# Kernel tuning notes

Measured on AMD Instinct MI355X. Metric: run time of the kernel, lower is better.

The kernel has to match this reference:

```python
import jax, jax.numpy as jnp
import numpy as np
from jax.ops import segment_sum, segment_max

N, E, IN_DIM, HID, HEADS, B, ACTIONS = 16384, 262144, 512, 256, 4, 64, 32
NEG_SLOPE = 0.2  # PyG GATConv default leaky-relu slope


def setup_inputs() -> dict:
    key = jax.random.key(0)
    ks = jax.random.split(key, 12)
    x = jax.random.normal(ks[0], (N, IN_DIM), dtype=jnp.float32)
    edge_index = jax.random.randint(ks[1], (2, E), 0, N, dtype=jnp.int64)
    batch = jnp.sort(jax.random.randint(ks[2], (N,), 0, B, dtype=jnp.int64))
    s = 0.05
    return {
        "x": x,
        "edge_index": edge_index,
        "batch": batch,
        # SAGEConv: lin_l (neighbors, with bias) + lin_r (root, no bias)
        "sage_w_l": jax.random.normal(ks[3], (IN_DIM, HID), dtype=jnp.float32) * s,
        "sage_b_l": jnp.zeros((HID,), dtype=jnp.float32),
        "sage_w_r": jax.random.normal(ks[4], (IN_DIM, HID), dtype=jnp.float32) * s,
        # GATConv: shared lin, per-head attention vectors, output bias (concat=False)
        "gat_w": jax.random.normal(ks[5], (HID, HEADS * HID), dtype=jnp.float32) * s,
        "gat_att_src": jax.random.normal(ks[6], (HEADS, HID), dtype=jnp.float32) * s,
        "gat_att_dst": jax.random.normal(ks[7], (HEADS, HID), dtype=jnp.float32) * s,
        "gat_b": jnp.zeros((HID,), dtype=jnp.float32),
        # action head
        "head_w": jax.random.normal(ks[8], (HID, ACTIONS), dtype=jnp.float32) * s,
        "head_b": jnp.zeros((ACTIONS,), dtype=jnp.float32),
    }


def reference(x, edge_index, batch, sage_w_l, sage_b_l, sage_w_r,
              gat_w, gat_att_src, gat_att_dst, gat_b, head_w, head_b):
    src, dst = edge_index[0], edge_index[1]

    # ---- SAGEConv (mean aggregation): lin_l(mean_j x_j) + lin_r(x_i) ----
    agg = segment_sum(x[src], dst, num_segments=N)                 # [N, IN_DIM]
    deg = segment_sum(jnp.ones((E,), x.dtype), dst, num_segments=N)
    mean_nbr = agg / jnp.maximum(deg, 1.0)[:, None]
    h = mean_nbr @ sage_w_l + sage_b_l + x @ sage_w_r              # [N, HID]
    h = jax.nn.relu(h)
    # dropout is identity at inference (training=False)

    # ---- GATConv (adds self-loops, concat=False -> head average) ----
    loop = jnp.arange(N, dtype=src.dtype)
    si = jnp.concatenate([src, loop])                              # [E2]
    di = jnp.concatenate([dst, loop])
    g = (h @ gat_w).reshape(N, HEADS, HID)                         # [N, H, C]
    a_src = jnp.einsum('nhc,hc->nh', g, gat_att_src)               # [N, H]
    a_dst = jnp.einsum('nhc,hc->nh', g, gat_att_dst)
    logits = jax.nn.leaky_relu(a_src[si] + a_dst[di], NEG_SLOPE)   # [E2, H]
    m = segment_max(logits, di, num_segments=N)                    # per-target max
    ex = jnp.exp(logits - m[di])
    denom = segment_sum(ex, di, num_segments=N)
    alpha = ex / denom[di]                                         # [E2, H]
    out = segment_sum(g[si] * alpha[:, :, None], di, num_segments=N)  # [N, H, C]
    out = jax.nn.relu(out.mean(axis=1) + gat_b)                    # [N, HID]

    # ---- global mean pool + action head ----
    pooled = segment_sum(out, batch, num_segments=B)
    cnt = segment_sum(jnp.ones((N,), out.dtype), batch, num_segments=B)
    pooled = pooled / jnp.maximum(cnt, 1.0)[:, None]               # [B, HID]
    return pooled @ head_w + head_b                                # [B, ACTIONS]
```

## Files before the change

kernel.cpp:

```cpp
#include <hip/hip_runtime.h>
#include <math.h>

#define N_NODES 16384
#define N_EDGES 262144
#define IN_DIM  512
#define HID     256
#define HEADS   4
#define NBATCH  64
#define ACTIONS 32
#define NEG_SLOPE 0.2f

typedef __attribute__((ext_vector_type(8))) short short8;
typedef __attribute__((ext_vector_type(4))) float f32x4;

__device__ __forceinline__ float lrelu(float v) { return v > 0.f ? v : NEG_SLOPE * v; }

__device__ __forceinline__ unsigned short bf16_rne(float f) {
    union { float f; unsigned int u; } x; x.f = f;
    unsigned int u = x.u;
    unsigned int r = (u + 0x7FFFu + ((u >> 16) & 1u)) >> 16;
    return (unsigned short)r;
}

__device__ __forceinline__ float bf16_to_f32(unsigned short s) {
    union { unsigned int u; float f; } x; x.u = (unsigned int)s << 16;
    return x.f;
}

__device__ __forceinline__ float4 bf4_to_f4(ushort4 u) {
    return make_float4(bf16_to_f32(u.x), bf16_to_f32(u.y), bf16_to_f32(u.z), bf16_to_f32(u.w));
}

__device__ __forceinline__ void async_copy16(const unsigned short* g, unsigned short* l) {
    __builtin_amdgcn_global_load_lds(
        (const __attribute__((address_space(1))) unsigned int*)g,
        (__attribute__((address_space(3))) unsigned int*)l, 16, 0, 0);
}

#define NB_WLR  1024
#define NB_WSTK 1024
#define NB_WATT 8
#define NB_DEG  1024
#define NB_SETUP (NB_WLR + NB_WSTK + NB_WATT + NB_DEG)

__global__ __launch_bounds__(256) void setup_kernel(
        const float* __restrict__ wl, const float* __restrict__ wr, unsigned short* __restrict__ bt1,
        const float* __restrict__ gat_w, unsigned short* __restrict__ bt2,
        const float* __restrict__ att_src, const float* __restrict__ att_dst, float* __restrict__ watt,
        const int* __restrict__ ei, int* __restrict__ deg) {
    int bid = blockIdx.x, tid = threadIdx.x;
    if (bid < NB_WLR) {
        int idx = bid * 256 + tid;
        int j = idx >> 9;
        int k = idx & 511;
        float v = (j < HID) ? wl[k * HID + j] : wr[k * HID + (j - HID)];
        bt1[idx] = bf16_rne(v);
    } else if (bid < NB_WLR + NB_WSTK) {
        int idx = (bid - NB_WLR) * 256 + tid;
        int c = idx >> 10;
        int r = idx & 1023;
        int h = r >> 8;
        int k = r & 255;
        bt2[idx] = bf16_rne(gat_w[(size_t)k * (HEADS * HID) + h * HID + c]);
    } else if (bid < NB_WLR + NB_WSTK + NB_WATT) {
        int j = bid - NB_WLR - NB_WSTK;
        int c = tid;
        int hh = j & 3;
        const float* att = (j < 4) ? (att_src + hh * HID) : (att_dst + hh * HID);
        float s = 0.f;
        for (int cc = 0; cc < HID; cc++)
            s += gat_w[(size_t)c * (HEADS * HID) + hh * HID + cc] * att[cc];
        watt[j * HID + c] = s;
    } else {
        int e = (bid - NB_WLR - NB_WSTK - NB_WATT) * 256 + tid;
        if (e < N_EDGES) atomicAdd(&deg[ei[N_EDGES + e]], 1);
    }
}

__global__ __launch_bounds__(256) void scan_kernel(const int* __restrict__ deg,
                                                   int* __restrict__ row_start,
                                                   int* __restrict__ pos) {
    int t = threadIdx.x;
    int lane = t & 63, wv = t >> 6;
    int base = t * 64;
    int4 buf[16];
    int sum = 0;
#pragma unroll
    for (int i = 0; i < 16; i++) {
        buf[i] = ((const int4*)(deg + base))[i];
        sum += buf[i].x + buf[i].y + buf[i].z + buf[i].w;
    }
    int v = sum;
#pragma unroll
    for (int off = 1; off < 64; off <<= 1) {
        int u = __shfl_up(v, off);
        if (lane >= off) v += u;
    }
    __shared__ int wsum[4];
    if (lane == 63) wsum[wv] = v;
    __syncthreads();
    int wbase = 0;
    for (int w0 = 0; w0 < wv; w0++) wbase += wsum[w0];
    int run = wbase + v - sum;
#pragma unroll
    for (int i = 0; i < 16; i++) {
        int4 b = buf[i];
        int4 o;
        o.x = run; run += b.x;
        o.y = run; run += b.y;
        o.z = run; run += b.z;
        o.w = run; run += b.w;
        ((int4*)(row_start + base))[i] = o;
        ((int4*)(pos + base))[i] = o;
    }
    if (t == 255) row_start[N_NODES] = run;
}

__global__ void fill_kernel(const int* __restrict__ ei, int* __restrict__ pos,
                            int* __restrict__ col) {
    int e = blockIdx.x * 256 + threadIdx.x;
    if (e < N_EDGES) {
        int s = ei[e];
        int d = ei[N_EDGES + e];
        int p = atomicAdd(&pos[d], 1);
        col[p] = s;
    }
}

#define BK 32

__global__ __launch_bounds__(256) void gemm1_kernel(const float* __restrict__ X,
                                                    const unsigned short* __restrict__ Bt,
                                                    unsigned short* __restrict__ Cb,
                                                    int Nn, int K) {
    __shared__ __align__(16) unsigned short As[2][2][64 * BK];
    __shared__ __align__(16) unsigned short Bs[2][2][128 * BK];

    int tid  = threadIdx.x;
    int wv   = tid >> 6;
    int lane = tid & 63;
    int m0 = blockIdx.y * 64;
    int n0 = blockIdx.x * 128;
    int wm = (wv & 1) * 32;
    int wn = (wv >> 1) * 64;

    int srow = tid >> 2;
    int scol = (tid & 3) * 8;
    const float*          Xg  = X  + (size_t)(m0 + srow) * K + scol;
    const unsigned short* Bg0 = Bt + (size_t)(n0 + srow) * K + scol;
    const unsigned short* Bg1 = Bt + (size_t)(n0 + 64 + srow) * K + scol;

    int fr = lane & 15;
    int fk = (lane >> 4) * 8;
    f32x4 acc[2][4] = {};
    float4 pa0[2], pa1[2];

#pragma unroll
    for (int s = 0; s < 2; s++) {
        int ko = s * BK;
        async_copy16(Bg0 + ko, &Bs[0][s][wv * 512]);
        async_copy16(Bg1 + ko, &Bs[0][s][2048 + wv * 512]);
        pa0[s] = *(const float4*)(Xg + ko);
        pa1[s] = *(const float4*)(Xg + ko + 4);
    }
#pragma unroll
    for (int s = 0; s < 2; s++) {
        short8 p;
        p[0] = (short)bf16_rne(pa0[s].x); p[1] = (short)bf16_rne(pa0[s].y);
        p[2] = (short)bf16_rne(pa0[s].z); p[3] = (short)bf16_rne(pa0[s].w);
        p[4] = (short)bf16_rne(pa1[s].x); p[5] = (short)bf16_rne(pa1[s].y);
        p[6] = (short)bf16_rne(pa1[s].z); p[7] = (short)bf16_rne(pa1[s].w);
        *(short8*)&As[0][s][srow * BK + scol] = p;
    }
    __syncthreads();

    int cur = 0;
    for (int kt = 0; kt < K; kt += 2 * BK) {
        int nxt = kt + 2 * BK;
        bool pf = nxt < K;
        if (pf) {
#pragma unroll
            for (int s = 0; s < 2; s++) {
                int ko = nxt + s * BK;
                async_copy16(Bg0 + ko, &Bs[cur ^ 1][s][wv * 512]);
                async_copy16(Bg1 + ko, &Bs[cur ^ 1][s][2048 + wv * 512]);
                pa0[s] = *(const float4*)(Xg + ko);
                pa1[s] = *(const float4*)(Xg + ko + 4);
            }
        }

#pragma unroll
        for (int s = 0; s < 2; s++) {
            short8 af[2], bf[4];
#pragma unroll
            for (int mi = 0; mi < 2; mi++)
                af[mi] = *(const short8*)&As[cur][s][(wm + mi * 16 + fr) * BK + fk];
#pragma unroll
            for (int ni = 0; ni < 4; ni++)
                bf[ni] = *(const short8*)&Bs[cur][s][(wn + ni * 16 + fr) * BK + fk];
#pragma unroll
            for (int mi = 0; mi < 2; mi++)
#pragma unroll
                for (int ni = 0; ni < 4; ni++)
                    acc[mi][ni] = __builtin_amdgcn_mfma_f32_16x16x32_bf16(af[mi], bf[ni], acc[mi][ni], 0, 0, 0);
        }

        if (pf) {
#pragma unroll
            for (int s = 0; s < 2; s++) {
                short8 p;
                p[0] = (short)bf16_rne(pa0[s].x); p[1] = (short)bf16_rne(pa0[s].y);
                p[2] = (short)bf16_rne(pa0[s].z); p[3] = (short)bf16_rne(pa0[s].w);
                p[4] = (short)bf16_rne(pa1[s].x); p[5] = (short)bf16_rne(pa1[s].y);
                p[6] = (short)bf16_rne(pa1[s].z); p[7] = (short)bf16_rne(pa1[s].w);
                *(short8*)&As[cur ^ 1][s][srow * BK + scol] = p;
            }
        }
        __syncthreads();
        cur ^= 1;
    }

    int cr = (lane >> 4) * 4;
    int cc = lane & 15;
#pragma unroll
    for (int mi = 0; mi < 2; mi++) {
#pragma unroll
        for (int ni = 0; ni < 4; ni++) {
            int gc = n0 + wn + ni * 16 + cc;
#pragma unroll
            for (int r = 0; r < 4; r++) {
                int gr = m0 + wm + mi * 16 + cr + r;
                Cb[(size_t)gr * Nn + gc] = bf16_rne(acc[mi][ni][r]);
            }
        }
    }
}

__global__ __launch_bounds__(256) void gemm2_pool_kernel(const unsigned short* __restrict__ A,
                                                         const unsigned short* __restrict__ Bt,
                                                         const int* __restrict__ batch,
                                                         const float* __restrict__ bias,
                                                         float scale,
                                                         float* __restrict__ pooled,
                                                         int Nn, int K) {
    __shared__ __align__(16) unsigned short As[2][2][64 * BK];
    __shared__ __align__(16) unsigned short Bs[2][2][64 * BK];
    __shared__ int bsh[64];

    int tid  = threadIdx.x;
    int wv   = tid >> 6;
    int lane = tid & 63;
    int m0 = blockIdx.y * 64;
    int n0 = blockIdx.x * 64;
    int wm = (wv & 1) * 32;
    int wn = (wv >> 1) * 32;

    if (tid < 64) bsh[tid] = batch[m0 + tid];

    int srow = tid >> 2;
    int scol = (tid & 3) * 8;
    const unsigned short* Ag = A  + (size_t)(m0 + srow) * K + scol;
    const unsigned short* Bg = Bt + (size_t)(n0 + srow) * K + scol;

    int fr = lane & 15;
    int fk = (lane >> 4) * 8;
    f32x4 acc[2][2] = {};

#pragma unroll
    for (int s = 0; s < 2; s++) {
        int ko = s * BK;
        async_copy16(Ag + ko, &As[0][s][wv * 512]);
        async_copy16(Bg + ko, &Bs[0][s][wv * 512]);
    }
    __syncthreads();

    int cur = 0;
    for (int kt = 0; kt < K; kt += 2 * BK) {
        int nxt = kt + 2 * BK;
        bool pf = nxt < K;
        if (pf) {
#pragma unroll
            for (int s = 0; s < 2; s++) {
                int ko = nxt + s * BK;
                async_copy16(Ag + ko, &As[cur ^ 1][s][wv * 512]);
                async_copy16(Bg + ko, &Bs[cur ^ 1][s][wv * 512]);
            }
        }

#pragma unroll
        for (int s = 0; s < 2; s++) {
            short8 af[2], bf[2];
#pragma unroll
            for (int mi = 0; mi < 2; mi++)
                af[mi] = *(const short8*)&As[cur][s][(wm + mi * 16 + fr) * BK + fk];
#pragma unroll
            for (int ni = 0; ni < 2; ni++)
                bf[ni] = *(const short8*)&Bs[cur][s][(wn + ni * 16 + fr) * BK + fk];
#pragma unroll
            for (int mi = 0; mi < 2; mi++)
#pragma unroll
                for (int ni = 0; ni < 2; ni++)
                    acc[mi][ni] = __builtin_amdgcn_mfma_f32_16x16x32_bf16(af[mi], bf[ni], acc[mi][ni], 0, 0, 0);
        }
        __syncthreads();
        cur ^= 1;
    }

    int cr = (lane >> 4) * 4;
    int cc = lane & 15;
#pragma unroll
    for (int mi = 0; mi < 2; mi++) {
        int rowb = wm + mi * 16 + cr;
        int b0 = bsh[rowb], b3 = bsh[rowb + 3];
#pragma unroll
        for (int ni = 0; ni < 2; ni++) {
            int gc = n0 + wn + ni * 16 + cc;
            float b = bias[gc];
            float v0 = fmaxf(fmaf(acc[mi][ni][0], scale, b), 0.f);
            float v1 = fmaxf(fmaf(acc[mi][ni][1], scale, b), 0.f);
            float v2 = fmaxf(fmaf(acc[mi][ni][2], scale, b), 0.f);
            float v3 = fmaxf(fmaf(acc[mi][ni][3], scale, b), 0.f);
            if (b0 == b3) {
                atomicAdd(&pooled[b0 * HID + gc], (v0 + v1) + (v2 + v3));
            } else {
                atomicAdd(&pooled[bsh[rowb + 0] * HID + gc], v0);
                atomicAdd(&pooled[bsh[rowb + 1] * HID + gc], v1);
                atomicAdd(&pooled[bsh[rowb + 2] * HID + gc], v2);
                atomicAdd(&pooled[bsh[rowb + 3] * HID + gc], v3);
            }
        }
    }
}

__global__ __launch_bounds__(256) void sage_agg_kernel(const unsigned short* __restrict__ xlr,
                                                       const int* __restrict__ row_start,
                                                       const int* __restrict__ col,
                                                       const float* __restrict__ b_l,
                                                       const float* __restrict__ watt,
                                                       unsigned short* __restrict__ hb,
                                                       float* __restrict__ a_att) {
    __shared__ float watt_s[8 * HID];
    for (int i = threadIdx.x; i < 8 * HID; i += 256) watt_s[i] = watt[i];
    __syncthreads();

    int wave = threadIdx.x >> 6;
    int lane = threadIdx.x & 63;
    int n = blockIdx.x * 4 + wave;
    int start = row_start[n], end = row_start[n + 1];
    int c0 = lane * 4;

    float4 acc = make_float4(0.f, 0.f, 0.f, 0.f);
    int e = start;
    for (; e + 4 <= end; e += 4) {
        int s0 = col[e], s1 = col[e + 1], s2 = col[e + 2], s3 = col[e + 3];
        ushort4 u0 = *(const ushort4*)(xlr + (size_t)s0 * IN_DIM + c0);
        ushort4 u1 = *(const ushort4*)(xlr + (size_t)s1 * IN_DIM + c0);
        ushort4 u2 = *(const ushort4*)(xlr + (size_t)s2 * IN_DIM + c0);
        ushort4 u3 = *(const ushort4*)(xlr + (size_t)s3 * IN_DIM + c0);
        float4 v0 = bf4_to_f4(u0), v1 = bf4_to_f4(u1), v2 = bf4_to_f4(u2), v3 = bf4_to_f4(u3);
        acc.x += (v0.x + v1.x) + (v2.x + v3.x);
        acc.y += (v0.y + v1.y) + (v2.y + v3.y);
        acc.z += (v0.z + v1.z) + (v2.z + v3.z);
        acc.w += (v0.w + v1.w) + (v2.w + v3.w);
    }
    for (; e < end; e++) {
        int s = col[e];
        float4 v = bf4_to_f4(*(const ushort4*)(xlr + (size_t)s * IN_DIM + c0));
        acc.x += v.x; acc.y += v.y; acc.z += v.z; acc.w += v.w;
    }
    float inv = 1.f / (float)max(end - start, 1);
    float4 xr = bf4_to_f4(*(const ushort4*)(xlr + (size_t)n * IN_DIM + HID + c0));
    float4 bl = *(const float4*)(b_l + c0);
    float4 hv;
    hv.x = fmaxf(fmaf(acc.x, inv, bl.x + xr.x), 0.f);
    hv.y = fmaxf(fmaf(acc.y, inv, bl.y + xr.y), 0.f);
    hv.z = fmaxf(fmaf(acc.z, inv, bl.z + xr.z), 0.f);
    hv.w = fmaxf(fmaf(acc.w, inv, bl.w + xr.w), 0.f);
    ushort4 ho;
    ho.x = bf16_rne(hv.x); ho.y = bf16_rne(hv.y); ho.z = bf16_rne(hv.z); ho.w = bf16_rne(hv.w);
    *(ushort4*)(hb + (size_t)n * HID + c0) = ho;

    float p[8];
#pragma unroll
    for (int j = 0; j < 8; j++) {
        float4 wt = *(const float4*)&watt_s[j * HID + c0];
        p[j] = hv.x * wt.x + hv.y * wt.y + hv.z * wt.z + hv.w * wt.w;
    }
#pragma unroll
    for (int off = 32; off; off >>= 1)
#pragma unroll
        for (int j = 0; j < 8; j++) p[j] += __shfl_down(p[j], off);
    if (lane == 0) {
#pragma unroll
        for (int j = 0; j < 8; j++) a_att[n * 8 + j] = p[j];
    }
}

__global__ __launch_bounds__(256) void gat_agg_kernel(const unsigned short* __restrict__ hb,
                                                      const float* __restrict__ a_att,
                                                      const int* __restrict__ row_start,
                                                      const int* __restrict__ col,
                                                      unsigned short* __restrict__ T) {
    __shared__ __align__(16) float w_s[4][64 * 4];
    int wave = threadIdx.x >> 6;
    int lane = threadIdx.x & 63;
    int n = blockIdx.x * 4 + wave;
    int start = row_start[n], end = row_start[n + 1];

    float4 an = *(const float4*)(a_att + n * 8);
    float4 ad = *(const float4*)(a_att + n * 8 + 4);
    float adst[4] = {ad.x, ad.y, ad.z, ad.w};
    float selfl[4] = {lrelu(an.x + ad.x), lrelu(an.y + ad.y), lrelu(an.z + ad.z), lrelu(an.w + ad.w)};
    float m[4], wself[4];
#pragma unroll
    for (int hh = 0; hh < 4; hh++) {
        m[hh] = fmaxf(selfl[hh], 0.f);
        wself[hh] = __expf(selfl[hh] - m[hh]);
    }

    int c0 = lane * 4;
    float4 hn = bf4_to_f4(*(const ushort4*)(hb + (size_t)n * HID + c0));
    float4 acc[4];
#pragma unroll
    for (int hh = 0; hh < 4; hh++)
        acc[hh] = make_float4(wself[hh] * hn.x, wself[hh] * hn.y, wself[hh] * hn.z, wself[hh] * hn.w);

    float dpart[4] = {0.f, 0.f, 0.f, 0.f};

    for (int base = start; base < end; base += 64) {
        int cnt = min(64, end - base);
        if (lane < cnt) {
            int s = col[base + lane];
            float4 as = *(const float4*)(a_att + s * 8);
            float4 wv;
            wv.x = __expf(lrelu(as.x + adst[0]) - m[0]);
            wv.y = __expf(lrelu(as.y + adst[1]) - m[1]);
            wv.z = __expf(lrelu(as.z + adst[2]) - m[2]);
            wv.w = __expf(lrelu(as.w + adst[3]) - m[3]);
            *(float4*)&w_s[wave][lane * 4] = wv;
            dpart[0] += wv.x; dpart[1] += wv.y; dpart[2] += wv.z; dpart[3] += wv.w;
        }
        __builtin_amdgcn_wave_barrier();

        int i = 0;
        for (; i + 2 <= cnt; i += 2) {
            int s0 = col[base + i], s1 = col[base + i + 1];
            float4 w0 = *(const float4*)&w_s[wave][i * 4];
            float4 w1 = *(const float4*)&w_s[wave][(i + 1) * 4];
            ushort4 u0 = *(const ushort4*)(hb + (size_t)s0 * HID + c0);
            ushort4 u1 = *(const ushort4*)(hb + (size_t)s1 * HID + c0);
            float4 h0 = bf4_to_f4(u0), h1 = bf4_to_f4(u1);
            float wr0[4] = {w0.x, w0.y, w0.z, w0.w};
            float wr1[4] = {w1.x, w1.y, w1.z, w1.w};
#pragma unroll
            for (int hh = 0; hh < 4; hh++) {
                acc[hh].x = fmaf(wr0[hh], h0.x, fmaf(wr1[hh], h1.x, acc[hh].x));
                acc[hh].y = fmaf(wr0[hh], h0.y, fmaf(wr1[hh], h1.y, acc[hh].y));
                acc[hh].z = fmaf(wr0[hh], h0.z, fmaf(wr1[hh], h1.z, acc[hh].z));
                acc[hh].w = fmaf(wr0[hh], h0.w, fmaf(wr1[hh], h1.w, acc[hh].w));
            }
        }
        if (i < cnt) {
            int s0 = col[base + i];
            float4 w0 = *(const float4*)&w_s[wave][i * 4];
            float4 h0 = bf4_to_f4(*(const ushort4*)(hb + (size_t)s0 * HID + c0));
            float wr0[4] = {w0.x, w0.y, w0.z, w0.w};
#pragma unroll
            for (int hh = 0; hh < 4; hh++) {
                acc[hh].x = fmaf(wr0[hh], h0.x, acc[hh].x);
                acc[hh].y = fmaf(wr0[hh], h0.y, acc[hh].y);
                acc[hh].z = fmaf(wr0[hh], h0.z, acc[hh].z);
                acc[hh].w = fmaf(wr0[hh], h0.w, acc[hh].w);
            }
        }
        __builtin_amdgcn_wave_barrier();
    }

#pragma unroll
    for (int off = 32; off; off >>= 1)
#pragma unroll
        for (int hh = 0; hh < 4; hh++) dpart[hh] += __shfl_down(dpart[hh], off);
    float invd[4];
#pragma unroll
    for (int hh = 0; hh < 4; hh++)
        invd[hh] = 1.f / (__shfl(dpart[hh], 0) + wself[hh]);

#pragma unroll
    for (int hh = 0; hh < 4; hh++) {
        ushort4 o;
        o.x = bf16_rne(acc[hh].x * invd[hh]); o.y = bf16_rne(acc[hh].y * invd[hh]);
        o.z = bf16_rne(acc[hh].z * invd[hh]); o.w = bf16_rne(acc[hh].w * invd[hh]);
        *(ushort4*)(T + (size_t)n * (HEADS * HID) + hh * HID + c0) = o;
    }
}

__device__ __forceinline__ int lower_bound_i(const int* a, int n, int v) {
    int lo = 0, hi = n;
    while (lo < hi) {
        int mid = (lo + hi) >> 1;
        if (a[mid] < v) lo = mid + 1; else hi = mid;
    }
    return lo;
}

__global__ __launch_bounds__(256) void head_kernel(const float* __restrict__ pooled,
                                                   const int* __restrict__ batch,
                                                   const float* __restrict__ head_w,
                                                   const float* __restrict__ head_b,
                                                   float* __restrict__ out) {
    __shared__ float sm[HID];
    int b = blockIdx.x;
    int c = threadIdx.x;
    int lo = lower_bound_i(batch, N_NODES, b);
    int hi = lower_bound_i(batch, N_NODES, b + 1);
    int cnt = hi - lo;
    sm[c] = pooled[b * HID + c] / (float)max(cnt, 1);
    __syncthreads();
    if (c < ACTIONS) {
        float acc = head_b[c];
        for (int k = 0; k < HID; k++) acc = fmaf(sm[k], head_w[k * ACTIONS + c], acc);
        out[b * ACTIONS + c] = acc;
    }
}

extern "C" void kernel_launch(void* const* d_in, const int* in_sizes, int n_in,
                              void* d_out, int out_size, void* d_ws, size_t ws_size,
                              hipStream_t stream) {
    const float* x        = (const float*)d_in[0];
    const int*   ei       = (const int*)d_in[1];
    const int*   batch    = (const int*)d_in[2];
    const float* sage_w_l = (const float*)d_in[3];
    const float* sage_b_l = (const float*)d_in[4];
    const float* sage_w_r = (const float*)d_in[5];
    const float* gat_w    = (const float*)d_in[6];
    const float* att_src  = (const float*)d_in[7];
    const float* att_dst  = (const float*)d_in[8];
    const float* gat_b    = (const float*)d_in[9];
    const float* head_w   = (const float*)d_in[10];
    const float* head_b   = (const float*)d_in[11];
    float* out = (float*)d_out;

    char* w = (char*)d_ws;
    int*   deg    = (int*)w;   w += (size_t)N_NODES * 4;
    float* pooled = (float*)w; w += (size_t)NBATCH * HID * 4;
    size_t zero_bytes = (size_t)N_NODES * 4 + (size_t)NBATCH * HID * 4;
    float* a_att  = (float*)w; w += (size_t)N_NODES * 8 * 4;
    float* watt   = (float*)w; w += (size_t)8 * HID * 4;
    unsigned short* xlr = (unsigned short*)w; w += (size_t)N_NODES * IN_DIM * 2;
    unsigned short* hb  = (unsigned short*)w; w += (size_t)N_NODES * HID * 2;
    unsigned short* T   = (unsigned short*)w; w += (size_t)N_NODES * HEADS * HID * 2;
    unsigned short* bt1 = (unsigned short*)w; w += (size_t)(2 * HID) * IN_DIM * 2;
    unsigned short* bt2 = (unsigned short*)w; w += (size_t)HID * (HEADS * HID) * 2;
    int* row_start= (int*)w;   w += (size_t)(N_NODES + 64) * 4;
    int* pos      = (int*)w;   w += (size_t)N_NODES * 4;
    int* col      = (int*)w;   w += (size_t)N_EDGES * 4;

    hipMemsetAsync(d_ws, 0, zero_bytes, stream);

    setup_kernel<<<NB_SETUP, 256, 0, stream>>>(sage_w_l, sage_w_r, bt1,
                                               gat_w, bt2, att_src, att_dst, watt,
                                               ei, deg);

    scan_kernel<<<1, 256, 0, stream>>>(deg, row_start, pos);
    fill_kernel<<<N_EDGES / 256, 256, 0, stream>>>(ei, pos, col);

    gemm1_kernel<<<dim3((2 * HID) / 128, N_NODES / 64), 256, 0, stream>>>(
        x, bt1, xlr, 2 * HID, IN_DIM);

    sage_agg_kernel<<<N_NODES / 4, 256, 0, stream>>>(xlr, row_start, col, sage_b_l, watt, hb, a_att);

    gat_agg_kernel<<<N_NODES / 4, 256, 0, stream>>>(hb, a_att, row_start, col, T);

    gemm2_pool_kernel<<<dim3(HID / 64, N_NODES / 64), 256, 0, stream>>>(
        T, bt2, batch, gat_b, 0.25f, pooled, HID, HEADS * HID);

    head_kernel<<<NBATCH, 256, 0, stream>>>(pooled, batch, head_w, head_b, out);
}
```

Baseline: 263.1 us.

## Pre-convert x to bf16 in setup and fuse action head into gemm2 tail

The fp32→bf16 conversion of x moves out of gemm1 and into a dedicated section of the setup kernel, writing into the T buffer before T is needed. This lets gemm1 stream A with async global-to-LDS copies, the same way it already loads B. The separate head kernel is removed. The last gemm2 block, found through an atomic counter, now computes the mean-pool division and the action-head matmul. This saves one launch but adds an extra pass over x and a serial tail done by a single block.

```diff
diff --git a/kernel.cpp b/kernel.cpp
--- a/kernel.cpp
+++ b/kernel.cpp
@@ -37,17 +37,19 @@
         (__attribute__((address_space(3))) unsigned int*)l, 16, 0, 0);
 }
 
-#define NB_WLR  1024
-#define NB_WSTK 1024
-#define NB_WATT 8
-#define NB_DEG  1024
-#define NB_SETUP (NB_WLR + NB_WSTK + NB_WATT + NB_DEG)
+#define NB_WLR   1024
+#define NB_WSTK  1024
+#define NB_WATT  8
+#define NB_DEG   1024
+#define NB_XCONV 4096
+#define NB_SETUP (NB_WLR + NB_WSTK + NB_WATT + NB_DEG + NB_XCONV)
 
 __global__ __launch_bounds__(256) void setup_kernel(
         const float* __restrict__ wl, const float* __restrict__ wr, unsigned short* __restrict__ bt1,
         const float* __restrict__ gat_w, unsigned short* __restrict__ bt2,
         const float* __restrict__ att_src, const float* __restrict__ att_dst, float* __restrict__ watt,
-        const int* __restrict__ ei, int* __restrict__ deg) {
+        const int* __restrict__ ei, int* __restrict__ deg,
+        const float* __restrict__ x, unsigned short* __restrict__ xb) {
     int bid = blockIdx.x, tid = threadIdx.x;
     if (bid < NB_WLR) {
         int idx = bid * 256 + tid;
@@ -71,9 +73,19 @@
         for (int cc = 0; cc < HID; cc++)
             s += gat_w[(size_t)c * (HEADS * HID) + hh * HID + cc] * att[cc];
         watt[j * HID + c] = s;
-    } else {
+    } else if (bid < NB_WLR + NB_WSTK + NB_WATT + NB_DEG) {
         int e = (bid - NB_WLR - NB_WSTK - NB_WATT) * 256 + tid;
         if (e < N_EDGES) atomicAdd(&deg[ei[N_EDGES + e]], 1);
+    } else {
+        size_t idx = (size_t)(bid - NB_WLR - NB_WSTK - NB_WATT - NB_DEG) * 2048 + (size_t)tid * 8;
+        float4 a0 = *(const float4*)(x + idx);
+        float4 a1 = *(const float4*)(x + idx + 4);
+        short8 p;
+        p[0] = (short)bf16_rne(a0.x); p[1] = (short)bf16_rne(a0.y);
+        p[2] = (short)bf16_rne(a0.z); p[3] = (short)bf16_rne(a0.w);
+        p[4] = (short)bf16_rne(a1.x); p[5] = (short)bf16_rne(a1.y);
+        p[6] = (short)bf16_rne(a1.z); p[7] = (short)bf16_rne(a1.w);
+        *(short8*)(xb + idx) = p;
     }
 }
 
@@ -129,7 +141,7 @@
 
 #define BK 32
 
-__global__ __launch_bounds__(256) void gemm1_kernel(const float* __restrict__ X,
+__global__ __launch_bounds__(256) void gemm1_kernel(const unsigned short* __restrict__ Ab,
                                                     const unsigned short* __restrict__ Bt,
                                                     unsigned short* __restrict__ Cb,
                                                     int Nn, int K) {
@@ -146,31 +158,20 @@
 
     int srow = tid >> 2;
     int scol = (tid & 3) * 8;
-    const float*          Xg  = X  + (size_t)(m0 + srow) * K + scol;
+    const unsigned short* Ag  = Ab + (size_t)(m0 + srow) * K + scol;
     const unsigned short* Bg0 = Bt + (size_t)(n0 + srow) * K + scol;
     const unsigned short* Bg1 = Bt + (size_t)(n0 + 64 + srow) * K + scol;
 
     int fr = lane & 15;
     int fk = (lane >> 4) * 8;
     f32x4 acc[2][4] = {};
-    float4 pa0[2], pa1[2];
 
 #pragma unroll
     for (int s = 0; s < 2; s++) {
         int ko = s * BK;
-        async_copy16(Bg0 + ko, &Bs[0][s][wv * 512]);
-        async_copy16(Bg1 + ko, &Bs[0][s][2048 + wv * 512]);
-        pa0[s] = *(const float4*)(Xg + ko);
-        pa1[s] = *(const float4*)(Xg + ko + 4);
-    }
-#pragma unroll
-    for (int s = 0; s < 2; s++) {
-        short8 p;
-        p[0] = (short)bf16_rne(pa0[s].x); p[1] = (short)bf16_rne(pa0[s].y);
-        p[2] = (short)bf16_rne(pa0[s].z); p[3] = (short)bf16_rne(pa0[s].w);
-        p[4] = (short)bf16_rne(pa1[s].x); p[5] = (short)bf16_rne(pa1[s].y);
-        p[6] = (short)bf16_rne(pa1[s].z); p[7] = (short)bf16_rne(pa1[s].w);
-        *(short8*)&As[0][s][srow * BK + scol] = p;
+        async_copy16(Ag + ko,      &As[0][s][wv * 512]);
+        async_copy16(Bg0 + ko,     &Bs[0][s][wv * 512]);
+        async_copy16(Bg1 + ko,     &Bs[0][s][2048 + wv * 512]);
     }
     __syncthreads();
 
@@ -182,10 +183,9 @@
 #pragma unroll
             for (int s = 0; s < 2; s++) {
                 int ko = nxt + s * BK;
+                async_copy16(Ag + ko,  &As[cur ^ 1][s][wv * 512]);
                 async_copy16(Bg0 + ko, &Bs[cur ^ 1][s][wv * 512]);
                 async_copy16(Bg1 + ko, &Bs[cur ^ 1][s][2048 + wv * 512]);
-                pa0[s] = *(const float4*)(Xg + ko);
-                pa1[s] = *(const float4*)(Xg + ko + 4);
             }
         }
 
@@ -203,18 +203,6 @@
 #pragma unroll
                 for (int ni = 0; ni < 4; ni++)
                     acc[mi][ni] = __builtin_amdgcn_mfma_f32_16x16x32_bf16(af[mi], bf[ni], acc[mi][ni], 0, 0, 0);
-        }
-
-        if (pf) {
-#pragma unroll
-            for (int s = 0; s < 2; s++) {
-                short8 p;
-                p[0] = (short)bf16_rne(pa0[s].x); p[1] = (short)bf16_rne(pa0[s].y);
-                p[2] = (short)bf16_rne(pa0[s].z); p[3] = (short)bf16_rne(pa0[s].w);
-                p[4] = (short)bf16_rne(pa1[s].x); p[5] = (short)bf16_rne(pa1[s].y);
-                p[6] = (short)bf16_rne(pa1[s].z); p[7] = (short)bf16_rne(pa1[s].w);
-                *(short8*)&As[cur ^ 1][s][srow * BK + scol] = p;
-            }
         }
         __syncthreads();
         cur ^= 1;
@@ -235,6 +223,17 @@
         }
     }
 }
+
+__device__ __forceinline__ int lower_bound_i(const int* a, int n, int v) {
+    int lo = 0, hi = n;
+    while (lo < hi) {
+        int mid = (lo + hi) >> 1;
+        if (a[mid] < v) lo = mid + 1; else hi = mid;
+    }
+    return lo;
+}
+
+#define G2_BLOCKS ((HID / 64) * (N_NODES / 64))
 
 __global__ __launch_bounds__(256) void gemm2_pool_kernel(const unsigned short* __restrict__ A,
                                                          const unsigned short* __restrict__ Bt,
@@ -242,6 +241,10 @@
                                                          const float* __restrict__ bias,
                                                          float scale,
                                                          float* __restrict__ pooled,
+                                                         int* __restrict__ counter,
+                                                         const float* __restrict__ head_w,
+                                                         const float* __restrict__ head_b,
+                                                         float* __restrict__ out,
                                                          int Nn, int K) {
     __shared__ __align__(16) unsigned short As[2][2][64 * BK];
     __shared__ __align__(16) unsigned short Bs[2][2][64 * BK];
@@ -330,6 +333,36 @@
             }
         }
     }
+
+    __threadfence();
+    __shared__ int lastflag;
+    if (tid == 0) {
+        int t = atomicAdd(counter, 1);
+        lastflag = (t == G2_BLOCKS - 1);
+    }
+    __syncthreads();
+    if (!lastflag) return;
+    __threadfence();
+
+    __shared__ int lb[NBATCH + 1];
+    if (tid <= NBATCH) lb[tid] = lower_bound_i(batch, N_NODES, tid);
+    __syncthreads();
+
+    int b  = tid >> 2;
+    int c0 = tid & 3;
+    float inv = 1.f / (float)max(lb[b + 1] - lb[b], 1);
+    float acch[8] = {0.f, 0.f, 0.f, 0.f, 0.f, 0.f, 0.f, 0.f};
+    for (int k = 0; k < HID; k++) {
+        float pv = __hip_atomic_load(&pooled[b * HID + k], __ATOMIC_RELAXED, __HIP_MEMORY_SCOPE_AGENT);
+#pragma unroll
+        for (int j = 0; j < 8; j++)
+            acch[j] = fmaf(pv, head_w[k * ACTIONS + c0 + 4 * j], acch[j]);
+    }
+#pragma unroll
+    for (int j = 0; j < 8; j++) {
+        int c = c0 + 4 * j;
+        out[b * ACTIONS + c] = fmaf(acch[j], inv, head_b[c]);
+    }
 }
 
 __global__ __launch_bounds__(256) void sage_agg_kernel(const unsigned short* __restrict__ xlr,
@@ -491,35 +524,6 @@
         o.x = bf16_rne(acc[hh].x * invd[hh]); o.y = bf16_rne(acc[hh].y * invd[hh]);
         o.z = bf16_rne(acc[hh].z * invd[hh]); o.w = bf16_rne(acc[hh].w * invd[hh]);
         *(ushort4*)(T + (size_t)n * (HEADS * HID) + hh * HID + c0) = o;
-    }
-}
-
-__device__ __forceinline__ int lower_bound_i(const int* a, int n, int v) {
-    int lo = 0, hi = n;
-    while (lo < hi) {
-        int mid = (lo + hi) >> 1;
-        if (a[mid] < v) lo = mid + 1; else hi = mid;
-    }
-    return lo;
-}
-
-__global__ __launch_bounds__(256) void head_kernel(const float* __restrict__ pooled,
-                                                   const int* __restrict__ batch,
-                                                   const float* __restrict__ head_w,
-                                                   const float* __restrict__ head_b,
-                                                   float* __restrict__ out) {
-    __shared__ float sm[HID];
-    int b = blockIdx.x;
-    int c = threadIdx.x;
-    int lo = lower_bound_i(batch, N_NODES, b);
-    int hi = lower_bound_i(batch, N_NODES, b + 1);
-    int cnt = hi - lo;
-    sm[c] = pooled[b * HID + c] / (float)max(cnt, 1);
-    __syncthreads();
-    if (c < ACTIONS) {
-        float acc = head_b[c];
-        for (int k = 0; k < HID; k++) acc = fmaf(sm[k], head_w[k * ACTIONS + c], acc);
-        out[b * ACTIONS + c] = acc;
     }
 }
 
@@ -541,9 +545,10 @@
     float* out = (float*)d_out;
 
     char* w = (char*)d_ws;
-    int*   deg    = (int*)w;   w += (size_t)N_NODES * 4;
-    float* pooled = (float*)w; w += (size_t)NBATCH * HID * 4;
-    size_t zero_bytes = (size_t)N_NODES * 4 + (size_t)NBATCH * HID * 4;
+    int*   deg     = (int*)w;   w += (size_t)N_NODES * 4;
+    float* pooled  = (float*)w; w += (size_t)NBATCH * HID * 4;
+    int*   counter = (int*)w;   w += 16;
+    size_t zero_bytes = (size_t)N_NODES * 4 + (size_t)NBATCH * HID * 4 + 16;
     float* a_att  = (float*)w; w += (size_t)N_NODES * 8 * 4;
     float* watt   = (float*)w; w += (size_t)8 * HID * 4;
     unsigned short* xlr = (unsigned short*)w; w += (size_t)N_NODES * IN_DIM * 2;
@@ -555,24 +560,24 @@
     int* pos      = (int*)w;   w += (size_t)N_NODES * 4;
     int* col      = (int*)w;   w += (size_t)N_EDGES * 4;
 
+    unsigned short* xb = T;
+
     hipMemsetAsync(d_ws, 0, zero_bytes, stream);
 
     setup_kernel<<<NB_SETUP, 256, 0, stream>>>(sage_w_l, sage_w_r, bt1,
                                                gat_w, bt2, att_src, att_dst, watt,
-                                               ei, deg);
+                                               ei, deg, x, xb);
 
     scan_kernel<<<1, 256, 0, stream>>>(deg, row_start, pos);
     fill_kernel<<<N_EDGES / 256, 256, 0, stream>>>(ei, pos, col);
 
     gemm1_kernel<<<dim3((2 * HID) / 128, N_NODES / 64), 256, 0, stream>>>(
-        x, bt1, xlr, 2 * HID, IN_DIM);
+        xb, bt1, xlr, 2 * HID, IN_DIM);
 
     sage_agg_kernel<<<N_NODES / 4, 256, 0, stream>>>(xlr, row_start, col, sage_b_l, watt, hb, a_att);
 
     gat_agg_kernel<<<N_NODES / 4, 256, 0, stream>>>(hb, a_att, row_start, col, T);
 
     gemm2_pool_kernel<<<dim3(HID / 64, N_NODES / 64), 256, 0, stream>>>(
-        T, bt2, batch, gat_b, 0.25f, pooled, HID, HEADS * HID);
-
-    head_kernel<<<NBATCH, 256, 0, stream>>>(pooled, batch, head_w, head_b, out);
-}
+        T, bt2, batch, gat_b, 0.25f, pooled, counter, head_w, head_b, out, HID, HEADS * HID);
+}
```

Result: slower. 378.2 us (+43.8%).
